# Kernel optimization log

Hardware: AMD Instinct MI355X
Metric: run time of the kernel (lower is better)

The kernel has to match this reference:

```python
import jax, jax.numpy as jnp
import numpy as np

HEADS = 8
K = 3            # kernel_size per axis
RPB = 2 * K - 1  # rel-pos-bias extent per axis
EPS = 1e-5


def _nbr(dim, k):
    # NATTEN-style clamped window: shift window to stay fully inside [0, dim)
    q = jnp.arange(dim)
    start = jnp.clip(q - k // 2, 0, dim - k)
    nbr = start[:, None] + jnp.arange(k)[None, :]       # (dim, k) neighbor coords
    rel = nbr - q[:, None] + (k - 1)                    # (dim, k) in [0, 2k-2]
    return nbr, rel


def _instance_norm(x):
    # InstanceNorm3d, affine=False: normalize over spatial dims per (B, C)
    m = jnp.mean(x, axis=(2, 3, 4), keepdims=True)
    v = jnp.var(x, axis=(2, 3, 4), keepdims=True)
    return (x - m) * jax.lax.rsqrt(v + EPS)


def setup_inputs() -> dict:
    key = jax.random.key(0)
    ks = jax.random.split(key, 10)
    B, C, H, W, Z = 1, 128, 32, 32, 32
    Cf = 4 * C
    s = 0.02
    return {
        "x": jax.random.normal(ks[0], (B, C, H, W, Z), jnp.float32),
        "w_qkv": jax.random.normal(ks[1], (3 * C, C), jnp.float32) * s,
        "b_qkv": jnp.zeros((3 * C,), jnp.float32),
        "rpb": jax.random.normal(ks[2], (HEADS, RPB, RPB, RPB), jnp.float32) * s,
        "w_proj": jax.random.normal(ks[3], (C, C), jnp.float32) * s,
        "b_proj": jnp.zeros((C,), jnp.float32),
        "w_ffn1": jax.random.normal(ks[4], (Cf, C), jnp.float32) * s,
        "b_ffn1": jnp.zeros((Cf,), jnp.float32),
        "w_ffn2": jax.random.normal(ks[5], (C, Cf), jnp.float32) * s,
        "b_ffn2": jnp.zeros((C,), jnp.float32),
    }


def reference(x, w_qkv, b_qkv, rpb, w_proj, b_proj, w_ffn1, b_ffn1, w_ffn2, b_ffn2):
    B, C, H, W, Z = x.shape
    hd = C // HEADS
    N = H * W * Z
    KK = K ** 3

    # ---- SAM: 3D neighborhood self-attention ----
    xt = x.reshape(B, C, N).transpose(0, 2, 1)                 # (B, N, C)
    qkv = xt @ w_qkv.T + b_qkv                                  # (B, N, 3C)
    q, k_, v = jnp.split(qkv, 3, axis=-1)
    split = lambda t: t.reshape(B, N, HEADS, hd).transpose(0, 2, 1, 3)  # (B, h, N, d)
    q, k_, v = split(q), split(k_), split(v)

    nh, rh = _nbr(H, K)
    nw, rw = _nbr(W, K)
    nz, rz = _nbr(Z, K)
    # flat neighbor token index per (h, w, z, kh, kw, kz)
    nbr = ((nh[:, None, None, :, None, None] * W
            + nw[None, :, None, None, :, None]) * Z
           + nz[None, None, :, None, None, :]).reshape(N, KK)   # (N, 27)
    # flat rel-pos-bias index
    bidx = ((rh[:, None, None, :, None, None] * RPB
             + rw[None, :, None, None, :, None]) * RPB
            + rz[None, None, :, None, None, :]).reshape(N, KK)  # (N, 27)

    kg = k_[:, :, nbr]                                          # (B, h, N, 27, d)
    vg = v[:, :, nbr]                                           # (B, h, N, 27, d)
    bias = rpb.reshape(HEADS, RPB ** 3)[:, bidx]                # (h, N, 27)

    scale = jnp.asarray(hd, x.dtype) ** -0.5
    attn = jnp.einsum('bhnd,bhnkd->bhnk', q * scale, kg) + bias
    attn = jax.nn.softmax(attn, axis=-1)
    out = jnp.einsum('bhnk,bhnkd->bhnd', attn, vg)              # (B, h, N, d)
    out = out.transpose(0, 2, 1, 3).reshape(B, N, C) @ w_proj.T + b_proj
    x5 = out.transpose(0, 2, 1).reshape(B, C, H, W, Z)

    # ---- norm_in ----
    x5 = _instance_norm(x5)

    # ---- FFN (mmcv-style, GELU, residual identity) ----
    t = x5.reshape(B, C, N).transpose(0, 2, 1)                  # (B, N, C)
    t = t + (jax.nn.gelu(t @ w_ffn1.T + b_ffn1) @ w_ffn2.T + b_ffn2)
    x5 = t.transpose(0, 2, 1).reshape(B, C, H, W, Z)

    # ---- norm_out ----
    return _instance_norm(x5)
```

## Files before the change

kernel.cpp:

```cpp
#include <hip/hip_runtime.h>
#include <hip/hip_bf16.h>
#include <math.h>

#define NPOS 32768
#define CCH  128
#define C3   384
#define CF   512
#define NSH  16

typedef __attribute__((ext_vector_type(8))) short short8;
typedef __attribute__((ext_vector_type(4))) float f32x4;

__device__ inline float bf2f(unsigned short u) {
    union { unsigned int i; float f; } x; x.i = ((unsigned int)u) << 16; return x.f;
}
__device__ inline unsigned short f2bf(float f) {
    union { float f; unsigned int i; } x; x.f = f;
    unsigned int r = x.i + 0x7FFFu + ((x.i >> 16) & 1u);
    return (unsigned short)(r >> 16);
}
__device__ inline float lo_bf(unsigned int u) {
    union { unsigned int i; float f; } x; x.i = u << 16; return x.f;
}
__device__ inline float hi_bf(unsigned int u) {
    union { unsigned int i; float f; } x; x.i = u & 0xffff0000u; return x.f;
}

__global__ __launch_bounds__(256) void qkv_fused_kernel(
    const float* __restrict__ x,
    const float* __restrict__ wqkv,
    const float* __restrict__ b_qkv,
    const float* __restrict__ wp,  const float* __restrict__ w1f,
    const float* __restrict__ w2f,
    unsigned short* __restrict__ wp_b, unsigned short* __restrict__ w1_b,
    unsigned short* __restrict__ w2_b,
    float* __restrict__ stats,
    unsigned short* __restrict__ outh)
{
    __shared__ alignas(16) unsigned short As[128 * 136];
    __shared__ alignas(16) unsigned short Bs[128 * 136];

    const int tid  = threadIdx.x;
    const int lane = tid & 63;
    const int wave = tid >> 6;
    const int wm = wave & 1, wn = wave >> 1;
    const int row0 = blockIdx.y * 128;
    const int col0 = blockIdx.x * 128;

    if (blockIdx.x == 0) {
        if (blockIdx.y < 16) {
            stats[blockIdx.y * 512 + tid] = 0.f;
            stats[blockIdx.y * 512 + 256 + tid] = 0.f;
        }
        if (tid < 144) {
            const int ci = blockIdx.y * 144 + tid;
            const float* src; unsigned short* dst; int off;
            if (ci < 4096)       { src = wp;  dst = wp_b; off = ci; }
            else if (ci < 20480) { src = w1f; dst = w1_b; off = ci - 4096; }
            else                 { src = w2f; dst = w2_b; off = ci - 20480; }
            const float4 v = ((const float4*)src)[off];
            ushort4 o;
            o.x = f2bf(v.x); o.y = f2bf(v.y); o.z = f2bf(v.z); o.w = f2bf(v.w);
            ((ushort4*)dst)[off] = o;
        }
    }

    #pragma unroll
    for (int it = 0; it < 16; ++it) {
        const int idx = tid + it * 256;
        const int c  = idx >> 5;
        const int nq = idx & 31;
        const float4 v = *(const float4*)&x[(size_t)c * NPOS + row0 + nq * 4];
        As[(nq * 4 + 0) * 136 + c] = f2bf(v.x);
        As[(nq * 4 + 1) * 136 + c] = f2bf(v.y);
        As[(nq * 4 + 2) * 136 + c] = f2bf(v.z);
        As[(nq * 4 + 3) * 136 + c] = f2bf(v.w);
    }
    #pragma unroll
    for (int it = 0; it < 16; ++it) {
        const int idx = tid + it * 256;
        const int col = idx >> 5;
        const int cq  = idx & 31;
        const float4 v = *(const float4*)&wqkv[(size_t)(col0 + col) * CCH + cq * 4];
        ushort4 o;
        o.x = f2bf(v.x); o.y = f2bf(v.y); o.z = f2bf(v.z); o.w = f2bf(v.w);
        *(ushort4*)&Bs[col * 136 + cq * 4] = o;
    }
    __syncthreads();

    const f32x4 fzero = {0.f, 0.f, 0.f, 0.f};
    f32x4 acc[4][4];
    #pragma unroll
    for (int i = 0; i < 4; ++i)
        #pragma unroll
        for (int j = 0; j < 4; ++j) acc[i][j] = fzero;

    const int lr = lane & 15;
    const int lk = (lane >> 4) * 8;

    #pragma unroll
    for (int ks = 0; ks < 4; ++ks) {
        short8 af[4], bfr[4];
        #pragma unroll
        for (int i = 0; i < 4; ++i)
            af[i]  = *(const short8*)&As[(wm * 64 + i * 16 + lr) * 136 + ks * 32 + lk];
        #pragma unroll
        for (int j = 0; j < 4; ++j)
            bfr[j] = *(const short8*)&Bs[(wn * 64 + j * 16 + lr) * 136 + ks * 32 + lk];
        #pragma unroll
        for (int i = 0; i < 4; ++i)
            #pragma unroll
            for (int j = 0; j < 4; ++j)
                acc[i][j] = __builtin_amdgcn_mfma_f32_16x16x32_bf16(
                                af[i], bfr[j], acc[i][j], 0, 0, 0);
    }

    const int gr0 = row0 + wm * 64 + (lane >> 4) * 4;
    const int gc0 = col0 + wn * 64 + lr;
    #pragma unroll
    for (int j = 0; j < 4; ++j) {
        const int gc  = gc0 + j * 16;
        const int sel = gc >> 4;
        const int ch  = gc & 15;
        const float bv = b_qkv[gc];
        #pragma unroll
        for (int i = 0; i < 4; ++i) {
            #pragma unroll
            for (int r = 0; r < 4; ++r) {
                const int gr = gr0 + i * 16 + r;
                outh[((size_t)sel * NPOS + gr) * 16 + ch] = f2bf(acc[i][j][r] + bv);
            }
        }
    }
}

__global__ __launch_bounds__(256) void attn_tiled(
    const unsigned short* __restrict__ qkv,
    const float* __restrict__ rpb,
    unsigned short* __restrict__ out)
{
    __shared__ unsigned int ksu[288 * 8];
    __shared__ unsigned int vsu[288 * 8];
    __shared__ unsigned int qsu[32 * 8];
    __shared__ float logits[32 * 29];
    __shared__ float rpbs[125];
    __shared__ float sinv[32];

    const int t  = threadIdx.x;
    const int line = ((blockIdx.x & 7) << 7) + (blockIdx.x >> 3);
    const int h  = blockIdx.y;
    const int w0 = line & 31, h0 = line >> 5;
    const int n0 = (h0 << 10) + (w0 << 5);
    const int sh0 = min(max(h0 - 1, 0), 29);
    const int sw0 = min(max(w0 - 1, 0), 29);
    const int rh_off = sh0 - h0 + 2;
    const int rw_off = sw0 - w0 + 2;

    if (t < 64) {
        const int pos = t >> 1, part = t & 1;
        const uint4 raw = *(const uint4*)&qkv[((size_t)h * NPOS + n0 + pos) * 16 + part * 8];
        *(uint4*)&qsu[pos * 8 + part * 4] = raw;
    } else if (t < 192) {
        const int i = t - 64;
        if (i < 125) rpbs[i] = rpb[h * 125 + i];
    }
    for (int c = t; c < 1152; c += 256) {
        const int p = c >> 2, part = c & 3;
        const int ihw = p >> 5, z = p & 31;
        const int ih = (ihw * 11) >> 5;
        const int iw = ihw - 3 * ih;
        const int n = ((sh0 + ih) << 10) + ((sw0 + iw) << 5) + z;
        const int kv = part >> 1;
        const uint4 raw = *(const uint4*)&qkv[((size_t)(8 + kv * 8 + h) * NPOS + n) * 16
                                              + (part & 1) * 8];
        unsigned int* d = ((kv == 0) ? ksu : vsu) + p * 8 + (part & 1) * 4;
        *(uint4*)d = raw;
    }
    __syncthreads();

    {
        const int q = t >> 3, j = t & 7;
        const int sz = min(max(q - 1, 0), 29);
        const int rz_off = sz - q + 2;
        float qf[16];
        #pragma unroll
        for (int d2 = 0; d2 < 8; ++d2) {
            const unsigned int u = qsu[q * 8 + d2];
            qf[2 * d2] = lo_bf(u); qf[2 * d2 + 1] = hi_bf(u);
        }
        float lv[4];
        int nkk = 0;
        for (int kk = j; kk < 27; kk += 8) {
            const int ihw = kk / 3, dz = kk - 3 * ihw;
            const int ih = ihw / 3,  iw = ihw - 3 * ih;
            const int p = ihw * 32 + sz + dz;
            float a = 0.f;
            #pragma unroll
            for (int d2 = 0; d2 < 8; ++d2) {
                const unsigned int u = ksu[p * 8 + d2];
                a += qf[2 * d2] * lo_bf(u) + qf[2 * d2 + 1] * hi_bf(u);
            }
            const int bidx = ((ih + rh_off) * 5 + (iw + rw_off)) * 5 + (dz + rz_off);
            lv[nkk++] = a * 0.25f + rpbs[bidx];
        }
        float mx = -1e30f;
        #pragma unroll
        for (int u = 0; u < 4; ++u) if (u < nkk) mx = fmaxf(mx, lv[u]);
        mx = fmaxf(mx, __shfl_xor(mx, 1));
        mx = fmaxf(mx, __shfl_xor(mx, 2));
        mx = fmaxf(mx, __shfl_xor(mx, 4));
        float s = 0.f;
        int u = 0;
        for (int kk = j; kk < 27; kk += 8) {
            const float e = __expf(lv[u++] - mx);
            logits[q * 29 + kk] = e;
            s += e;
        }
        s += __shfl_xor(s, 1);
        s += __shfl_xor(s, 2);
        s += __shfl_xor(s, 4);
        if (j == 0) sinv[q] = 1.f / s;
    }
    __syncthreads();

    {
        const int q = t >> 3, d2 = t & 7;
        const int sz = min(max(q - 1, 0), 29);
        float ax = 0.f, ay = 0.f;
        #pragma unroll
        for (int kk = 0; kk < 27; ++kk) {
            const int p = (kk / 3) * 32 + sz + (kk % 3);
            const float w = logits[q * 29 + kk];
            const unsigned int u = vsu[p * 8 + d2];
            ax += w * lo_bf(u); ay += w * hi_bf(u);
        }
        const float inv = sinv[q];
        const unsigned int o = ((unsigned int)f2bf(ay * inv) << 16)
                             |  (unsigned int)f2bf(ax * inv);
        *(unsigned int*)&out[(size_t)(n0 + q) * CCH + h * 16 + d2 * 2] = o;
    }
}

__global__ __launch_bounds__(256) void proj_stats_kernel(
    const unsigned short* __restrict__ attnO,
    const unsigned short* __restrict__ wproj,
    const float* __restrict__ b_proj,
    unsigned short* __restrict__ x5b,
    float* __restrict__ stats)
{
    __shared__ float red[256];

    const int t    = threadIdx.x;
    const int lane = t & 63;
    const int wn   = t >> 6;
    const int lr = lane & 15;
    const int lg = lane >> 4;
    const int lk = lg * 8;
    const int n0 = blockIdx.x * 64;
    const int sh = (blockIdx.x & (NSH - 1)) * 256;

    red[t] = 0.f;

    short8 wf[2][4];
    #pragma unroll
    for (int j = 0; j < 2; ++j)
        #pragma unroll
        for (int ks = 0; ks < 4; ++ks)
            wf[j][ks] = *(const short8*)&wproj[(wn * 32 + j * 16 + lr) * CCH + ks * 32 + lk];

    const f32x4 fzero = {0.f, 0.f, 0.f, 0.f};
    f32x4 acc[4][2];
    #pragma unroll
    for (int i = 0; i < 4; ++i)
        #pragma unroll
        for (int j = 0; j < 2; ++j) acc[i][j] = fzero;

    #pragma unroll
    for (int ks = 0; ks < 4; ++ks) {
        short8 af[4];
        #pragma unroll
        for (int i = 0; i < 4; ++i)
            af[i] = *(const short8*)&attnO[(size_t)(n0 + i * 16 + lr) * CCH + ks * 32 + lk];
        #pragma unroll
        for (int i = 0; i < 4; ++i)
            #pragma unroll
            for (int j = 0; j < 2; ++j)
                acc[i][j] = __builtin_amdgcn_mfma_f32_16x16x32_bf16(
                                af[i], wf[j][ks], acc[i][j], 0, 0, 0);
    }
    __syncthreads();

    #pragma unroll
    for (int j = 0; j < 2; ++j) {
        const int gc = wn * 32 + j * 16 + lr;
        const float bv = b_proj[gc];
        float s = 0.f, q = 0.f;
        #pragma unroll
        for (int i = 0; i < 4; ++i)
            #pragma unroll
            for (int r = 0; r < 4; ++r) {
                const int gr = i * 16 + lg * 4 + r;
                const float v = acc[i][j][r] + bv;
                s += v; q += v * v;
                x5b[(size_t)(n0 + gr) * CCH + gc] = f2bf(v);
            }
        atomicAdd(&red[gc], s);
        atomicAdd(&red[128 + gc], q);
    }
    __syncthreads();
    if (t < 128) {
        atomicAdd(&stats[sh + t],       red[t]);
        atomicAdd(&stats[sh + 128 + t], red[128 + t]);
    }
}

__global__ __launch_bounds__(256) void ffn_fused_kernel(
    const unsigned short* __restrict__ x5b,
    const unsigned short* __restrict__ w1,
    const float* __restrict__ b1,
    const unsigned short* __restrict__ w2,
    const float* __restrict__ b2,
    float* __restrict__ stats,
    unsigned short* __restrict__ tTb)
{
    __shared__ alignas(16) unsigned short pool[2 * 8704];
    unsigned short* As = pool;
    unsigned short* Hs = pool + 8704;
    __shared__ float red[256];
    __shared__ float ms[128];
    __shared__ float rss[128];

    const int t    = threadIdx.x;
    const int lane = t & 63;
    const int wn   = t >> 6;
    const int lr = lane & 15;
    const int lg = lane >> 4;
    const int lk = lg * 8;
    const int n0 = blockIdx.x * 64;
    const int sh = (blockIdx.x & (NSH - 1)) * 256;
    const float invN = 1.f / (float)NPOS;
    const f32x4 fzero = {0.f, 0.f, 0.f, 0.f};

    red[t] = 0.f;
    if (t < 128) {
        float s0 = 0.f, s1 = 0.f;
        #pragma unroll
        for (int s = 0; s < NSH; ++s) {
            s0 += stats[s * 256 + t];
            s1 += stats[s * 256 + 128 + t];
        }
        const float m = s0 * invN;
        const float v = s1 * invN - m * m;
        ms[t]  = m;
        rss[t] = rsqrtf(v + 1e-5f);
    }
    uint4 px[4];
    #pragma unroll
    for (int it = 0; it < 4; ++it) {
        const int idx = t + it * 256;
        const int row = idx >> 4, c0 = (idx & 15) * 8;
        px[it] = *(const uint4*)&x5b[(size_t)(n0 + row) * CCH + c0];
    }
    __syncthreads();

    #pragma unroll
    for (int it = 0; it < 4; ++it) {
        const int idx = t + it * 256;
        const int row = idx >> 4, c0 = (idx & 15) * 8;
        unsigned int u[4] = {px[it].x, px[it].y, px[it].z, px[it].w};
        #pragma unroll
        for (int p = 0; p < 4; ++p) {
            const int c = c0 + 2 * p;
            const float a = (lo_bf(u[p]) - ms[c])     * rss[c];
            const float b = (hi_bf(u[p]) - ms[c + 1]) * rss[c + 1];
            u[p] = ((unsigned int)f2bf(b) << 16) | (unsigned int)f2bf(a);
        }
        uint4 w; w.x = u[0]; w.y = u[1]; w.z = u[2]; w.w = u[3];
        *(uint4*)&As[row * 136 + c0] = w;
    }
    __syncthreads();

    f32x4 acc[4][2];
    #pragma unroll
    for (int i = 0; i < 4; ++i)
        #pragma unroll
        for (int j = 0; j < 2; ++j) acc[i][j] = fzero;

    #pragma unroll 1
    for (int cc = 0; cc < 4; ++cc) {
        short8 w1f[2][4];
        #pragma unroll
        for (int j = 0; j < 2; ++j)
            #pragma unroll
            for (int ks = 0; ks < 4; ++ks)
                w1f[j][ks] = *(const short8*)&w1[
                    (size_t)(cc * 128 + wn * 32 + j * 16 + lr) * CCH + ks * 32 + lk];

        f32x4 hacc[4][2];
        #pragma unroll
        for (int i = 0; i < 4; ++i)
            #pragma unroll
            for (int j = 0; j < 2; ++j) hacc[i][j] = fzero;
        #pragma unroll
        for (int ks = 0; ks < 4; ++ks) {
            short8 af[4];
            #pragma unroll
            for (int i = 0; i < 4; ++i)
                af[i] = *(const short8*)&As[(i * 16 + lr) * 136 + ks * 32 + lk];
            #pragma unroll
            for (int i = 0; i < 4; ++i)
                #pragma unroll
                for (int j = 0; j < 2; ++j)
                    hacc[i][j] = __builtin_amdgcn_mfma_f32_16x16x32_bf16(
                                    af[i], w1f[j][ks], hacc[i][j], 0, 0, 0);
        }

        short8 w2f[2][4];
        #pragma unroll
        for (int j = 0; j < 2; ++j)
            #pragma unroll
            for (int ks = 0; ks < 4; ++ks)
                w2f[j][ks] = *(const short8*)&w2[
                    (size_t)(wn * 32 + j * 16 + lr) * CF + cc * 128 + ks * 32 + lk];

        #pragma unroll
        for (int j = 0; j < 2; ++j) {
            const int gc = wn * 32 + j * 16 + lr;
            const float bv = b1[cc * 128 + gc];
            #pragma unroll
            for (int i = 0; i < 4; ++i)
                #pragma unroll
                for (int r = 0; r < 4; ++r) {
                    float v = hacc[i][j][r] + bv;
                    const float g = 0.7978845608028654f * (v + 0.044715f * v * v * v);
                    const float e = __expf(2.f * g);
                    v = v * (e / (e + 1.f));
                    Hs[(i * 16 + lg * 4 + r) * 136 + gc] = f2bf(v);
                }
        }
        __syncthreads();

        #pragma unroll
        for (int ks = 0; ks < 4; ++ks) {
            short8 af[4];
            #pragma unroll
            for (int i = 0; i < 4; ++i)
                af[i] = *(const short8*)&Hs[(i * 16 + lr) * 136 + ks * 32 + lk];
            #pragma unroll
            for (int i = 0; i < 4; ++i)
                #pragma unroll
                for (int j = 0; j < 2; ++j)
                    acc[i][j] = __builtin_amdgcn_mfma_f32_16x16x32_bf16(
                                    af[i], w2f[j][ks], acc[i][j], 0, 0, 0);
        }
        __syncthreads();
    }

    #pragma unroll
    for (int j = 0; j < 2; ++j) {
        const int gc = wn * 32 + j * 16 + lr;
        const float bv = b2[gc];
        float s = 0.f, q = 0.f;
        #pragma unroll
        for (int i = 0; i < 4; ++i)
            #pragma unroll
            for (int r = 0; r < 4; ++r) {
                const int gr = i * 16 + lg * 4 + r;
                const float v = acc[i][j][r] + bv + bf2f(As[gr * 136 + gc]);
                acc[i][j][r] = v;
                s += v; q += v * v;
            }
        atomicAdd(&red[gc], s);
        atomicAdd(&red[128 + gc], q);
    }
    __syncthreads();
    if (t < 128) {
        atomicAdd(&stats[4096 + sh + t],       red[t]);
        atomicAdd(&stats[4096 + sh + 128 + t], red[128 + t]);
    }

    float* tr = (float*)pool;
    #pragma unroll
    for (int j = 0; j < 2; ++j) {
        const int gc = wn * 32 + j * 16 + lr;
        #pragma unroll
        for (int i = 0; i < 4; ++i)
            #pragma unroll
            for (int r = 0; r < 4; ++r) {
                const int gr = i * 16 + lg * 4 + r;
                tr[gc * 68 + gr] = acc[i][j][r];
            }
    }
    __syncthreads();
    #pragma unroll
    for (int it = 0; it < 8; ++it) {
        const int idx = t + it * 256;
        const int c = idx >> 4, ch = (idx & 15) * 4;
        ushort4 o4;
        o4.x = f2bf(tr[c * 68 + ch + 0]);
        o4.y = f2bf(tr[c * 68 + ch + 1]);
        o4.z = f2bf(tr[c * 68 + ch + 2]);
        o4.w = f2bf(tr[c * 68 + ch + 3]);
        *(ushort4*)&tTb[(size_t)c * NPOS + n0 + ch] = o4;
    }
}

__global__ __launch_bounds__(256) void norm2_apply_kernel(
    const unsigned short* __restrict__ tTb, const float* __restrict__ stats,
    float* __restrict__ out)
{
    const int i = blockIdx.x * 256 + threadIdx.x;
    const size_t o = (size_t)i * 8;
    const int c = (int)(o >> 15);
    const float invN = 1.f / (float)NPOS;
    float s0 = 0.f, s1 = 0.f;
    #pragma unroll
    for (int s = 0; s < NSH; ++s) {
        s0 += stats[4096 + s * 256 + c];
        s1 += stats[4096 + s * 256 + 128 + c];
    }
    const float m  = s0 * invN;
    const float vr = s1 * invN - m * m;
    const float rs = rsqrtf(vr + 1e-5f);
    const uint4 raw = *(const uint4*)&tTb[o];
    const unsigned int u[4] = {raw.x, raw.y, raw.z, raw.w};
    float4 o0, o1;
    o0.x = (lo_bf(u[0]) - m) * rs; o0.y = (hi_bf(u[0]) - m) * rs;
    o0.z = (lo_bf(u[1]) - m) * rs; o0.w = (hi_bf(u[1]) - m) * rs;
    o1.x = (lo_bf(u[2]) - m) * rs; o1.y = (hi_bf(u[2]) - m) * rs;
    o1.z = (lo_bf(u[3]) - m) * rs; o1.w = (hi_bf(u[3]) - m) * rs;
    *(float4*)&out[o]     = o0;
    *(float4*)&out[o + 4] = o1;
}

extern "C" void kernel_launch(void* const* d_in, const int* in_sizes, int n_in,
                              void* d_out, int out_size, void* d_ws, size_t ws_size,
                              hipStream_t stream)
{
    const float* x      = (const float*)d_in[0];
    const float* w_qkv  = (const float*)d_in[1];
    const float* b_qkv  = (const float*)d_in[2];
    const float* rpb    = (const float*)d_in[3];
    const float* w_proj = (const float*)d_in[4];
    const float* b_proj = (const float*)d_in[5];
    const float* w_ffn1 = (const float*)d_in[6];
    const float* b_ffn1 = (const float*)d_in[7];
    const float* w_ffn2 = (const float*)d_in[8];
    const float* b_ffn2 = (const float*)d_in[9];
    float* out = (float*)d_out;

    char* ws = (char*)d_ws;
    unsigned short* qkv_bf   = (unsigned short*)(ws + 8388608);
    unsigned short* attnO_bf = (unsigned short*)(ws + 33554432);
    unsigned short* x5_bf    = (unsigned short*)(ws + 41943040);
    unsigned short* tTb      = (unsigned short*)(ws + 50331648);
    unsigned short* wproj_bf = (unsigned short*)(ws + 83984384);
    unsigned short* wffn1_bf = (unsigned short*)(ws + 84017152);
    unsigned short* wffn2_bf = (unsigned short*)(ws + 84148224);
    float*          stats    = (float*)(ws + 84279296);

    qkv_fused_kernel<<<dim3(C3 / 128, NPOS / 128), 256, 0, stream>>>(
        x, w_qkv, b_qkv, w_proj, w_ffn1, w_ffn2,
        wproj_bf, wffn1_bf, wffn2_bf, stats, qkv_bf);

    attn_tiled<<<dim3(1024, 8), 256, 0, stream>>>(qkv_bf, rpb, attnO_bf);

    proj_stats_kernel<<<NPOS / 64, 256, 0, stream>>>(
        attnO_bf, wproj_bf, b_proj, x5_bf, stats);

    ffn_fused_kernel<<<NPOS / 64, 256, 0, stream>>>(
        x5_bf, wffn1_bf, b_ffn1, wffn2_bf, b_ffn2, stats, tTb);

    norm2_apply_kernel<<<(NPOS * CCH / 8) / 256, 256, 0, stream>>>(tTb, stats, out);
}
```

Measured before the change: 178.3 us.

## Tile attention over 2x2 z-lines per block to share K/V halo loads

Each attention block now handles a 2x2 patch of (h,w) lines, 128 queries, instead of one line of 32. It loads a shared 4x4x32 K/V halo into LDS. This cuts redundant global K/V loads from 9 lines per query line to 16 lines per 4 query lines. The cost is more LDS per block (about 50KB), fewer blocks (2048), and serial loops over 4 sub-batches of queries, which may reduce occupancy.

```diff
diff --git a/kernel.cpp b/kernel.cpp
--- a/kernel.cpp
+++ b/kernel.cpp
@@ -139,37 +139,41 @@
     const float* __restrict__ rpb,
     unsigned short* __restrict__ out)
 {
-    __shared__ unsigned int ksu[288 * 8];
-    __shared__ unsigned int vsu[288 * 8];
-    __shared__ unsigned int qsu[32 * 8];
-    __shared__ float logits[32 * 29];
+    __shared__ unsigned int ksu[512 * 8];
+    __shared__ unsigned int vsu[512 * 8];
+    __shared__ unsigned int qsu[128 * 8];
+    __shared__ float logits[128 * 29];
     __shared__ float rpbs[125];
-    __shared__ float sinv[32];
+    __shared__ float sinv[128];
 
     const int t  = threadIdx.x;
-    const int line = ((blockIdx.x & 7) << 7) + (blockIdx.x >> 3);
+    const int patch = ((blockIdx.x & 7) << 5) + (blockIdx.x >> 3);
     const int h  = blockIdx.y;
-    const int w0 = line & 31, h0 = line >> 5;
-    const int n0 = (h0 << 10) + (w0 << 5);
-    const int sh0 = min(max(h0 - 1, 0), 29);
-    const int sw0 = min(max(w0 - 1, 0), 29);
-    const int rh_off = sh0 - h0 + 2;
-    const int rw_off = sw0 - w0 + 2;
-
-    if (t < 64) {
+    const int ph = patch >> 4, pw = patch & 15;
+    const int hb = min(max(2 * ph - 1, 0), 28);
+    const int wb = min(max(2 * pw - 1, 0), 28);
+
+    {
         const int pos = t >> 1, part = t & 1;
-        const uint4 raw = *(const uint4*)&qkv[((size_t)h * NPOS + n0 + pos) * 16 + part * 8];
+        const int lsel = pos >> 5;
+        const int z = pos & 31;
+        const int h0l = 2 * ph + (lsel >> 1);
+        const int w0l = 2 * pw + (lsel & 1);
+        const int n = (h0l << 10) + (w0l << 5) + z;
+        const uint4 raw = *(const uint4*)&qkv[((size_t)h * NPOS + n) * 16 + part * 8];
         *(uint4*)&qsu[pos * 8 + part * 4] = raw;
-    } else if (t < 192) {
-        const int i = t - 64;
-        if (i < 125) rpbs[i] = rpb[h * 125 + i];
-    }
-    for (int c = t; c < 1152; c += 256) {
+    }
+    if (t < 125) rpbs[t] = rpb[h * 125 + t];
+
+    #pragma unroll
+    for (int it = 0; it < 8; ++it) {
+        const int c = t + it * 256;
         const int p = c >> 2, part = c & 3;
-        const int ihw = p >> 5, z = p & 31;
-        const int ih = (ihw * 11) >> 5;
-        const int iw = ihw - 3 * ih;
-        const int n = ((sh0 + ih) << 10) + ((sw0 + iw) << 5) + z;
+        const int ihh = p >> 7;
+        const int rem = p & 127;
+        const int iww = rem >> 5;
+        const int z   = rem & 31;
+        const int n = ((hb + ihh) << 10) + ((wb + iww) << 5) + z;
         const int kv = part >> 1;
         const uint4 raw = *(const uint4*)&qkv[((size_t)(8 + kv * 8 + h) * NPOS + n) * 16
                                               + (part & 1) * 8];
@@ -178,10 +182,23 @@
     }
     __syncthreads();
 
-    {
-        const int q = t >> 3, j = t & 7;
-        const int sz = min(max(q - 1, 0), 29);
-        const int rz_off = sz - q + 2;
+    #pragma unroll 1
+    for (int s = 0; s < 4; ++s) {
+        const int q = (t >> 3) + s * 32;
+        const int j = t & 7;
+        const int lsel = q >> 5;
+        const int z = q & 31;
+        const int h0l = 2 * ph + (lsel >> 1);
+        const int w0l = 2 * pw + (lsel & 1);
+        const int sh0 = min(max(h0l - 1, 0), 29);
+        const int sw0 = min(max(w0l - 1, 0), 29);
+        const int ih_off = sh0 - hb;
+        const int iw_off = sw0 - wb;
+        const int rh_off = sh0 - h0l + 2;
+        const int rw_off = sw0 - w0l + 2;
+        const int sz = min(max(z - 1, 0), 29);
+        const int rz_off = sz - z + 2;
+
         float qf[16];
         #pragma unroll
         for (int d2 = 0; d2 < 8; ++d2) {
@@ -193,7 +210,7 @@
         for (int kk = j; kk < 27; kk += 8) {
             const int ihw = kk / 3, dz = kk - 3 * ihw;
             const int ih = ihw / 3,  iw = ihw - 3 * ih;
-            const int p = ihw * 32 + sz + dz;
+            const int p = ((ih_off + ih) * 4 + (iw_off + iw)) * 32 + sz + dz;
             float a = 0.f;
             #pragma unroll
             for (int d2 = 0; d2 < 8; ++d2) {
@@ -209,27 +226,41 @@
         mx = fmaxf(mx, __shfl_xor(mx, 1));
         mx = fmaxf(mx, __shfl_xor(mx, 2));
         mx = fmaxf(mx, __shfl_xor(mx, 4));
-        float s = 0.f;
+        float sm = 0.f;
         int u = 0;
         for (int kk = j; kk < 27; kk += 8) {
             const float e = __expf(lv[u++] - mx);
             logits[q * 29 + kk] = e;
-            s += e;
-        }
-        s += __shfl_xor(s, 1);
-        s += __shfl_xor(s, 2);
-        s += __shfl_xor(s, 4);
-        if (j == 0) sinv[q] = 1.f / s;
-    }
-    __syncthreads();
-
-    {
-        const int q = t >> 3, d2 = t & 7;
-        const int sz = min(max(q - 1, 0), 29);
+            sm += e;
+        }
+        sm += __shfl_xor(sm, 1);
+        sm += __shfl_xor(sm, 2);
+        sm += __shfl_xor(sm, 4);
+        if (j == 0) sinv[q] = 1.f / sm;
+    }
+    __syncthreads();
+
+    #pragma unroll 1
+    for (int s = 0; s < 4; ++s) {
+        const int q = (t >> 3) + s * 32;
+        const int d2 = t & 7;
+        const int lsel = q >> 5;
+        const int z = q & 31;
+        const int h0l = 2 * ph + (lsel >> 1);
+        const int w0l = 2 * pw + (lsel & 1);
+        const int sh0 = min(max(h0l - 1, 0), 29);
+        const int sw0 = min(max(w0l - 1, 0), 29);
+        const int ih_off = sh0 - hb;
+        const int iw_off = sw0 - wb;
+        const int sz = min(max(z - 1, 0), 29);
+        const int n = (h0l << 10) + (w0l << 5) + z;
+
         float ax = 0.f, ay = 0.f;
         #pragma unroll
         for (int kk = 0; kk < 27; ++kk) {
-            const int p = (kk / 3) * 32 + sz + (kk % 3);
+            const int ihw = kk / 3, dz = kk - 3 * ihw;
+            const int ih = ihw / 3,  iw = ihw - 3 * ih;
+            const int p = ((ih_off + ih) * 4 + (iw_off + iw)) * 32 + sz + dz;
             const float w = logits[q * 29 + kk];
             const unsigned int u = vsu[p * 8 + d2];
             ax += w * lo_bf(u); ay += w * hi_bf(u);
@@ -237,7 +268,7 @@
         const float inv = sinv[q];
         const unsigned int o = ((unsigned int)f2bf(ay * inv) << 16)
                              |  (unsigned int)f2bf(ax * inv);
-        *(unsigned int*)&out[(size_t)(n0 + q) * CCH + h * 16 + d2 * 2] = o;
+        *(unsigned int*)&out[(size_t)n * CCH + h * 16 + d2 * 2] = o;
     }
 }
 
@@ -563,7 +594,7 @@
         x, w_qkv, b_qkv, w_proj, w_ffn1, w_ffn2,
         wproj_bf, wffn1_bf, wffn2_bf, stats, qkv_bf);
 
-    attn_tiled<<<dim3(1024, 8), 256, 0, stream>>>(qkv_bf, rpb, attnO_bf);
+    attn_tiled<<<dim3(256, 8), 256, 0, stream>>>(qkv_bf, rpb, attnO_bf);
 
     proj_stats_kernel<<<NPOS / 64, 256, 0, stream>>>(
         attnO_bf, wproj_bf, b_proj, x5_bf, stats);
```

Result: slower. 183.0 us (+2.6%).
